# Optimization experiments

Measured on AMD Instinct MI355X. Metric: run time of the kernel, lower is better.

Reference implementation:

```python
import jax, jax.numpy as jnp
import numpy as np

SPC = 8                                   # samples_per_class
SIG_TEMP = 0.01                           # sigmoid_temperature
K_VALS = (1.0, 2.0, 4.0, 8.0, 16.0)       # all <= batch_size so min(batch,k)=k
K_TEMPS = (1.0, 2.0, 4.0, 8.0, 16.0)


def _sig(x, temp):
    # faithful to original: clamp exponent to [-50, 50]
    e = jnp.clip(-x / temp, -50.0, 50.0)
    return 1.0 / (1.0 + jnp.exp(e))


def setup_inputs() -> dict:
    key = jax.random.key(0)
    preds = jax.random.normal(key, (2048, 1024), dtype=jnp.float32)
    # embeddings are typically L2-normalized before this loss
    preds = preds / jnp.linalg.norm(preds, axis=1, keepdims=True)
    return {"preds": preds, "q_idx": 0}


def reference(preds, q_idx):
    B = preds.shape[0]
    spc = SPC
    kv = jnp.asarray(K_VALS, preds.dtype)          # [K]
    kt = jnp.asarray(K_TEMPS, preds.dtype)         # [K]
    norm_vals = jnp.minimum(kv, float(spc - 1))    # [K]

    idx = jnp.arange(B)
    g = idx // spc            # group id of each query
    r = idx % spc             # position of query within its group

    # all pairwise similarities: S[q, j] = <preds[q], preds[j]>
    S = preds @ preds.T                                        # [B, B]

    # G[q, i] = sim of query q with i-th member of q's own group
    cols = g[:, None] * spc + jnp.arange(spc)[None, :]         # [B, spc]
    G = jnp.take_along_axis(S, cols, axis=1)                   # [B, spc]

    # sim_diff_all[q, j, i] = S[q, j] - G[q, i]
    sg = _sig(S[:, :, None] - G[:, None, :], SIG_TEMP)         # [B, B, spc]

    # zero sim_sg[q, g(q)*spc + i, i]
    jr = jnp.arange(B)[None, :, None]
    ir = jnp.arange(spc)[None, None, :]
    diag_mask = jr == (g[:, None, None] * spc + ir)            # [B, B, spc]
    sg = jnp.where(diag_mask, 0.0, sg)

    # surrogate rank of each in-group sample w.r.t. query q
    rk = 1.0 + sg.sum(axis=1)                                  # [B, spc]
    self_mask = jnp.arange(spc)[None, :] == r[:, None]         # [B, spc]
    rk = jnp.where(self_mask, 0.0, rk)

    # per-k sigmoid indicator rank <= k
    v = _sig(kv[None, None, :] - rk[:, :, None], kt[None, None, :])  # [B, spc, K]
    v = jnp.where(self_mask[:, :, None], 0.0, v)

    recall = jnp.minimum(v.sum(axis=1), kv[None, :]) / norm_vals[None, :]  # [B, K]
    recall_q = recall.mean(axis=1)                                         # [B]
    return jnp.mean(1.0 - recall_q)
```

## Files before the change

### kernel.cpp

```cpp
#include <hip/hip_runtime.h>

#define BATCH 2048
#define DIM   1024
#define SPC   8
#define BM    128
#define BN    64
#define BK    32
#define NKT   (DIM / BK)
#define NJB   (BATCH / BN)

typedef _Float16 half8  __attribute__((ext_vector_type(8)));
typedef _Float16 half4v __attribute__((ext_vector_type(4)));
typedef float    f32x4  __attribute__((ext_vector_type(4)));

constexpr float INV_T    = 1.0f / 0.01f;
constexpr float LO_SCALE = 2048.0f;
constexpr float INV_LO   = 1.0f / 2048.0f;

__device__ __forceinline__ float sig_main(float x) {
  float e = -x * INV_T;
  e = fminf(fmaxf(e, -50.0f), 50.0f);
  return 1.0f / (1.0f + __expf(e));
}

__device__ __forceinline__ void gl_lds16(const _Float16* g, _Float16* l) {
  __builtin_amdgcn_global_load_lds((const __attribute__((address_space(1))) void*)g,
                                   (__attribute__((address_space(3))) void*)l, 16, 0, 0);
}

__device__ __forceinline__ int swz(int row, int c) { return row * 4 + (c ^ ((row >> 1) & 3)); }

__global__ __launch_bounds__(256) void k_prep(const float* __restrict__ preds,
                                              _Float16* __restrict__ Ph,
                                              _Float16* __restrict__ Pl,
                                              float* __restrict__ G) {
  __shared__ float rows[SPC][DIM + 4];
  __shared__ float part[64][4];
  if (blockIdx.x < BATCH) {
    const int i = blockIdx.x * 256 + threadIdx.x;
    const float4 x = ((const float4*)preds)[i];
    half4v h, l;
    h[0] = (_Float16)x.x; l[0] = (_Float16)((x.x - (float)h[0]) * LO_SCALE);
    h[1] = (_Float16)x.y; l[1] = (_Float16)((x.y - (float)h[1]) * LO_SCALE);
    h[2] = (_Float16)x.z; l[2] = (_Float16)((x.z - (float)h[2]) * LO_SCALE);
    h[3] = (_Float16)x.w; l[3] = (_Float16)((x.w - (float)h[3]) * LO_SCALE);
    ((half4v*)Ph)[i] = h;
    ((half4v*)Pl)[i] = l;
    return;
  }
  const int g = blockIdx.x - BATCH;
  const int tid = threadIdx.x;
  const float4* src = (const float4*)(preds + (size_t)g * SPC * DIM);
#pragma unroll
  for (int c = 0; c < 8; ++c) {
    int idx = c * 256 + tid;
    float4 v = src[idx];
    *(float4*)&rows[idx >> 8][(idx & 255) << 2] = v;
  }
  __syncthreads();
  const int p  = tid & 63;
  const int sl = tid >> 6;
  const float4* ra = (const float4*)&rows[p >> 3][sl * 256];
  const float4* rb = (const float4*)&rows[p & 7][sl * 256];
  float s = 0.0f;
#pragma unroll 8
  for (int e = 0; e < 64; ++e) {
    float4 a = ra[e], b = rb[e];
    s += a.x * b.x + a.y * b.y + a.z * b.z + a.w * b.w;
  }
  part[p][sl] = s;
  __syncthreads();
  if (tid < 64) {
    float v = part[tid][0] + part[tid][1] + part[tid][2] + part[tid][3];
    G[(size_t)(g * SPC + (tid >> 3)) * SPC + (tid & 7)] = v;
  }
}

__global__ __launch_bounds__(256, 2) void k_main(const _Float16* __restrict__ Ph,
                                                 const _Float16* __restrict__ Pl,
                                                 const float* __restrict__ G,
                                                 float* __restrict__ partial) {
  __shared__ __align__(16) _Float16 sAh0[BM * BK], sAl0[BM * BK], sBh0[BN * BK], sBl0[BN * BK];
  __shared__ __align__(16) _Float16 sAh1[BM * BK], sAl1[BM * BK], sBh1[BN * BK], sBl1[BN * BK];
  __shared__ float sRed[2][BM][SPC];
  const int t    = threadIdx.x;
  const int lane = t & 63;
  const int w    = t >> 6;
  const int wr   = w >> 1, wc = w & 1;

  int bid = blockIdx.y * gridDim.x + blockIdx.x;
  bid = (bid & 7) * (512 / 8) + (bid >> 3);
  const int qb    = (bid / NJB) * BM;
  const int jbIdx = bid % NJB;
  const int jb    = jbIdx * BN;

  f32x4 accH[4][2], accX[4][2];
#pragma unroll
  for (int m = 0; m < 4; ++m)
#pragma unroll
    for (int n = 0; n < 2; ++n) {
      accH[m][n] = (f32x4){0.f, 0.f, 0.f, 0.f};
      accX[m][n] = (f32x4){0.f, 0.f, 0.f, 0.f};
    }

  auto STAGE = [&](_Float16* dAh, _Float16* dAl, _Float16* dBh, _Float16* dBl, int kt) {
    const int kk = kt * BK;
#pragma unroll
    for (int e = 0; e < 2; ++e) {
      const int slot = e * 256 + t;
      const int row  = slot >> 2;
      const int c    = (slot & 3) ^ ((row >> 1) & 3);
      const size_t src = (size_t)(qb + row) * DIM + kk + c * 8;
      gl_lds16(Ph + src, dAh + (size_t)slot * 8);
      gl_lds16(Pl + src, dAl + (size_t)slot * 8);
    }
    {
      const int slot = t;
      const int row  = slot >> 2;
      const int c    = (slot & 3) ^ ((row >> 1) & 3);
      const size_t src = (size_t)(jb + row) * DIM + kk + c * 8;
      gl_lds16(Ph + src, dBh + (size_t)slot * 8);
      gl_lds16(Pl + src, dBl + (size_t)slot * 8);
    }
  };

  const int rl = lane & 15, ch = lane >> 4;
  auto COMPUTE = [&](const _Float16* bAh, const _Float16* bAl,
                     const _Float16* bBh, const _Float16* bBl) {
    half8 ah[4], al[4], bh[2], bl[2];
#pragma unroll
    for (int m = 0; m < 4; ++m) {
      const int r = wr * 64 + m * 16 + rl;
      const int s = swz(r, ch);
      ah[m] = *(const half8*)&bAh[(size_t)s * 8];
      al[m] = *(const half8*)&bAl[(size_t)s * 8];
    }
#pragma unroll
    for (int n = 0; n < 2; ++n) {
      const int r = wc * 32 + n * 16 + rl;
      const int s = swz(r, ch);
      bh[n] = *(const half8*)&bBh[(size_t)s * 8];
      bl[n] = *(const half8*)&bBl[(size_t)s * 8];
    }
#pragma unroll
    for (int m = 0; m < 4; ++m)
#pragma unroll
      for (int n = 0; n < 2; ++n) {
        accH[m][n] = __builtin_amdgcn_mfma_f32_16x16x32_f16(ah[m], bh[n], accH[m][n], 0, 0, 0);
        accX[m][n] = __builtin_amdgcn_mfma_f32_16x16x32_f16(ah[m], bl[n], accX[m][n], 0, 0, 0);
        accX[m][n] = __builtin_amdgcn_mfma_f32_16x16x32_f16(al[m], bh[n], accX[m][n], 0, 0, 0);
      }
  };

  STAGE(sAh0, sAl0, sBh0, sBl0, 0);
  __syncthreads();
#pragma unroll 1
  for (int kt = 0; kt < NKT; kt += 2) {
    if (kt + 1 < NKT) STAGE(sAh1, sAl1, sBh1, sBl1, kt + 1);
    COMPUTE(sAh0, sAl0, sBh0, sBl0);
    __syncthreads();
    if (kt + 2 < NKT) STAGE(sAh0, sAl0, sBh0, sBl0, kt + 2);
    COMPUTE(sAh1, sAl1, sBh1, sBl1);
    __syncthreads();
  }

  const int colLane = lane & 15;
  const int rowLane = lane >> 4;
#pragma unroll
  for (int m = 0; m < 4; ++m) {
#pragma unroll
    for (int v = 0; v < 4; ++v) {
      const int q = qb + wr * 64 + m * 16 + rowLane * 4 + v;
      const float4 g0 = *(const float4*)&G[(size_t)q * 8];
      const float4 g1 = *(const float4*)&G[(size_t)q * 8 + 4];
      const float gv[8] = {g0.x, g0.y, g0.z, g0.w, g1.x, g1.y, g1.z, g1.w};
      const int qg = q >> 3;
      float sv[2];
      int jg[2], jp[2];
#pragma unroll
      for (int n = 0; n < 2; ++n) {
        sv[n] = accH[m][n][v] + accX[m][n][v] * INV_LO;
        const int j = jb + wc * 32 + n * 16 + colLane;
        jg[n] = j >> 3;
        jp[n] = j & 7;
      }
#pragma unroll
      for (int i = 0; i < 8; ++i) {
        float pr = 0.0f;
#pragma unroll
        for (int n = 0; n < 2; ++n) {
          float s = sig_main(sv[n] - gv[i]);
          if (jg[n] == qg && jp[n] == i) s = 0.0f;
          pr += s;
        }
        pr += __shfl_xor(pr, 1);
        pr += __shfl_xor(pr, 2);
        pr += __shfl_xor(pr, 4);
        pr += __shfl_xor(pr, 8);
        if (colLane == 0)
          sRed[wc][wr * 64 + m * 16 + rowLane * 4 + v][i] = pr;
      }
    }
  }
  __syncthreads();
  {
    const float* r0 = &sRed[0][0][0];
    const float* r1 = &sRed[1][0][0];
    float4 a = *(const float4*)&r0[t * 4];
    float4 b = *(const float4*)&r1[t * 4];
    float4 s = {a.x + b.x, a.y + b.y, a.z + b.z, a.w + b.w};
    *(float4*)&partial[((size_t)jbIdx * BATCH + qb) * SPC + t * 4] = s;
  }
}

__global__ __launch_bounds__(256) void k_fin(const float* __restrict__ partial,
                                             float* __restrict__ out) {
  const int q = blockIdx.x * 256 + threadIdx.x;
  float rk8[8] = {0.f, 0.f, 0.f, 0.f, 0.f, 0.f, 0.f, 0.f};
#pragma unroll 4
  for (int p = 0; p < NJB; ++p) {
    const float* base = &partial[((size_t)p * BATCH + q) * SPC];
    float4 a = *(const float4*)&base[0];
    float4 b = *(const float4*)&base[4];
    rk8[0] += a.x; rk8[1] += a.y; rk8[2] += a.z; rk8[3] += a.w;
    rk8[4] += b.x; rk8[5] += b.y; rk8[6] += b.z; rk8[7] += b.w;
  }
  const float kv[5]  = {1.f, 2.f, 4.f, 8.f, 16.f};
  const float rkt[5] = {1.f, 0.5f, 0.25f, 0.125f, 0.0625f};
  const float nv[5]  = {1.f, 2.f, 4.f, 7.f, 7.f};
  const int r = q & 7;
  float vs[5] = {0.f, 0.f, 0.f, 0.f, 0.f};
#pragma unroll
  for (int i = 0; i < 8; ++i) {
    const float rk = 1.0f + rk8[i];
    const bool self = (i == r);
#pragma unroll
    for (int k = 0; k < 5; ++k) {
      float e = (rk - kv[k]) * rkt[k];
      e = fminf(fmaxf(e, -50.0f), 50.0f);
      float v = 1.0f / (1.0f + __expf(e));
      vs[k] += self ? 0.0f : v;
    }
  }
  float rq = 0.0f;
#pragma unroll
  for (int k = 0; k < 5; ++k) rq += fminf(vs[k], kv[k]) / nv[k];
  float tv = (1.0f - rq * 0.2f) * (1.0f / (float)BATCH);
#pragma unroll
  for (int o = 1; o < 64; o <<= 1) tv += __shfl_xor(tv, o);
  if ((threadIdx.x & 63) == 0) atomicAdd(out, tv);
}

extern "C" void kernel_launch(void* const* d_in, const int* in_sizes, int n_in,
                              void* d_out, int out_size, void* d_ws, size_t ws_size,
                              hipStream_t stream) {
  const float* preds = (const float*)d_in[0];
  float* G       = (float*)d_ws;
  float* partial = (float*)((char*)d_ws + (64 << 10));
  _Float16* Ph   = (_Float16*)((char*)d_ws + (64 << 10) + (2 << 20));
  _Float16* Pl   = Ph + (size_t)BATCH * DIM;
  hipMemsetAsync(d_out, 0, sizeof(float), stream);
  k_prep<<<BATCH + BATCH / SPC, 256, 0, stream>>>(preds, Ph, Pl, G);
  k_main<<<dim3(BATCH / BN, BATCH / BM), 256, 0, stream>>>(Ph, Pl, G, partial);
  k_fin<<<BATCH / 256, 256, 0, stream>>>(partial, (float*)d_out);
}
```

Before: 131.0 us.

## Shrink main tile to 64x64, remap blocks per XCD, parallelize final reduction

```diff
diff --git a/kernel.cpp b/kernel.cpp
--- a/kernel.cpp
+++ b/kernel.cpp
@@ -3,7 +3,7 @@
 #define BATCH 2048
 #define DIM   1024
 #define SPC   8
-#define BM    128
+#define BM    64
 #define BN    64
 #define BK    32
 #define NKT   (DIM / BK)
@@ -17,10 +17,9 @@
 constexpr float LO_SCALE = 2048.0f;
 constexpr float INV_LO   = 1.0f / 2048.0f;
 
-__device__ __forceinline__ float sig_main(float x) {
-  float e = -x * INV_T;
-  e = fminf(fmaxf(e, -50.0f), 50.0f);
-  return 1.0f / (1.0f + __expf(e));
+__device__ __forceinline__ float sig_fast(float x) {
+  float e = fminf(fmaxf(-x * INV_T, -50.0f), 50.0f);
+  return __builtin_amdgcn_rcpf(1.0f + __expf(e));
 }
 
 __device__ __forceinline__ void gl_lds16(const _Float16* g, _Float16* l) {
@@ -76,7 +75,7 @@
   }
 }
 
-__global__ __launch_bounds__(256, 2) void k_main(const _Float16* __restrict__ Ph,
+__global__ __launch_bounds__(256, 4) void k_main(const _Float16* __restrict__ Ph,
                                                  const _Float16* __restrict__ Pl,
                                                  const float* __restrict__ G,
                                                  float* __restrict__ partial) {
@@ -88,15 +87,15 @@
   const int w    = t >> 6;
   const int wr   = w >> 1, wc = w & 1;
 
-  int bid = blockIdx.y * gridDim.x + blockIdx.x;
-  bid = (bid & 7) * (512 / 8) + (bid >> 3);
-  const int qb    = (bid / NJB) * BM;
-  const int jbIdx = bid % NJB;
+  const int d    = blockIdx.y * 32 + blockIdx.x;
+  const int xcd  = d & 7, idx = d >> 3;
+  const int jbIdx = xcd * 4 + (idx & 3);
+  const int qb    = (idx >> 2) * BM;
   const int jb    = jbIdx * BN;
 
-  f32x4 accH[4][2], accX[4][2];
-#pragma unroll
-  for (int m = 0; m < 4; ++m)
+  f32x4 accH[2][2], accX[2][2];
+#pragma unroll
+  for (int m = 0; m < 2; ++m)
 #pragma unroll
     for (int n = 0; n < 2; ++n) {
       accH[m][n] = (f32x4){0.f, 0.f, 0.f, 0.f};
@@ -104,46 +103,35 @@
     }
 
   auto STAGE = [&](_Float16* dAh, _Float16* dAl, _Float16* dBh, _Float16* dBl, int kt) {
-    const int kk = kt * BK;
-#pragma unroll
-    for (int e = 0; e < 2; ++e) {
-      const int slot = e * 256 + t;
-      const int row  = slot >> 2;
-      const int c    = (slot & 3) ^ ((row >> 1) & 3);
-      const size_t src = (size_t)(qb + row) * DIM + kk + c * 8;
-      gl_lds16(Ph + src, dAh + (size_t)slot * 8);
-      gl_lds16(Pl + src, dAl + (size_t)slot * 8);
-    }
-    {
-      const int slot = t;
-      const int row  = slot >> 2;
-      const int c    = (slot & 3) ^ ((row >> 1) & 3);
-      const size_t src = (size_t)(jb + row) * DIM + kk + c * 8;
-      gl_lds16(Ph + src, dBh + (size_t)slot * 8);
-      gl_lds16(Pl + src, dBl + (size_t)slot * 8);
-    }
+    const int kk  = kt * BK;
+    const int row = t >> 2;
+    const int c   = (t & 3) ^ ((row >> 1) & 3);
+    const size_t sA = (size_t)(qb + row) * DIM + kk + c * 8;
+    const size_t sB = (size_t)(jb + row) * DIM + kk + c * 8;
+    gl_lds16(Ph + sA, dAh + (size_t)t * 8);
+    gl_lds16(Pl + sA, dAl + (size_t)t * 8);
+    gl_lds16(Ph + sB, dBh + (size_t)t * 8);
+    gl_lds16(Pl + sB, dBl + (size_t)t * 8);
   };
 
   const int rl = lane & 15, ch = lane >> 4;
   auto COMPUTE = [&](const _Float16* bAh, const _Float16* bAl,
                      const _Float16* bBh, const _Float16* bBl) {
-    half8 ah[4], al[4], bh[2], bl[2];
-#pragma unroll
-    for (int m = 0; m < 4; ++m) {
-      const int r = wr * 64 + m * 16 + rl;
-      const int s = swz(r, ch);
+    half8 ah[2], al[2], bh[2], bl[2];
+#pragma unroll
+    for (int m = 0; m < 2; ++m) {
+      const int s = swz(wr * 32 + m * 16 + rl, ch);
       ah[m] = *(const half8*)&bAh[(size_t)s * 8];
       al[m] = *(const half8*)&bAl[(size_t)s * 8];
     }
 #pragma unroll
     for (int n = 0; n < 2; ++n) {
-      const int r = wc * 32 + n * 16 + rl;
-      const int s = swz(r, ch);
+      const int s = swz(wc * 32 + n * 16 + rl, ch);
       bh[n] = *(const half8*)&bBh[(size_t)s * 8];
       bl[n] = *(const half8*)&bBl[(size_t)s * 8];
     }
 #pragma unroll
-    for (int m = 0; m < 4; ++m)
+    for (int m = 0; m < 2; ++m)
 #pragma unroll
       for (int n = 0; n < 2; ++n) {
         accH[m][n] = __builtin_amdgcn_mfma_f32_16x16x32_f16(ah[m], bh[n], accH[m][n], 0, 0, 0);
@@ -167,10 +155,11 @@
   const int colLane = lane & 15;
   const int rowLane = lane >> 4;
 #pragma unroll
-  for (int m = 0; m < 4; ++m) {
+  for (int m = 0; m < 2; ++m) {
 #pragma unroll
     for (int v = 0; v < 4; ++v) {
-      const int q = qb + wr * 64 + m * 16 + rowLane * 4 + v;
+      const int ql = wr * 32 + m * 16 + rowLane * 4 + v;
+      const int q  = qb + ql;
       const float4 g0 = *(const float4*)&G[(size_t)q * 8];
       const float4 g1 = *(const float4*)&G[(size_t)q * 8 + 4];
       const float gv[8] = {g0.x, g0.y, g0.z, g0.w, g1.x, g1.y, g1.z, g1.w};
@@ -189,7 +178,7 @@
         float pr = 0.0f;
 #pragma unroll
         for (int n = 0; n < 2; ++n) {
-          float s = sig_main(sv[n] - gv[i]);
+          float s = sig_fast(sv[n] - gv[i]);
           if (jg[n] == qg && jp[n] == i) s = 0.0f;
           pr += s;
         }
@@ -197,13 +186,12 @@
         pr += __shfl_xor(pr, 2);
         pr += __shfl_xor(pr, 4);
         pr += __shfl_xor(pr, 8);
-        if (colLane == 0)
-          sRed[wc][wr * 64 + m * 16 + rowLane * 4 + v][i] = pr;
+        if (colLane == 0) sRed[wc][ql][i] = pr;
       }
     }
   }
   __syncthreads();
-  {
+  if (t < 128) {
     const float* r0 = &sRed[0][0][0];
     const float* r1 = &sRed[1][0][0];
     float4 a = *(const float4*)&r0[t * 4];
@@ -215,40 +203,41 @@
 
 __global__ __launch_bounds__(256) void k_fin(const float* __restrict__ partial,
                                              float* __restrict__ out) {
-  const int q = blockIdx.x * 256 + threadIdx.x;
-  float rk8[8] = {0.f, 0.f, 0.f, 0.f, 0.f, 0.f, 0.f, 0.f};
-#pragma unroll 4
-  for (int p = 0; p < NJB; ++p) {
-    const float* base = &partial[((size_t)p * BATCH + q) * SPC];
-    float4 a = *(const float4*)&base[0];
-    float4 b = *(const float4*)&base[4];
-    rk8[0] += a.x; rk8[1] += a.y; rk8[2] += a.z; rk8[3] += a.w;
-    rk8[4] += b.x; rk8[5] += b.y; rk8[6] += b.z; rk8[7] += b.w;
-  }
+  const int tg = blockIdx.x * 256 + threadIdx.x;
+  const int q = tg >> 3, i = tg & 7;
+  float rk = 1.0f;
+#pragma unroll 8
+  for (int p = 0; p < NJB; ++p)
+    rk += partial[(size_t)p * BATCH * SPC + tg];
   const float kv[5]  = {1.f, 2.f, 4.f, 8.f, 16.f};
   const float rkt[5] = {1.f, 0.5f, 0.25f, 0.125f, 0.0625f};
   const float nv[5]  = {1.f, 2.f, 4.f, 7.f, 7.f};
-  const int r = q & 7;
-  float vs[5] = {0.f, 0.f, 0.f, 0.f, 0.f};
-#pragma unroll
-  for (int i = 0; i < 8; ++i) {
-    const float rk = 1.0f + rk8[i];
-    const bool self = (i == r);
-#pragma unroll
-    for (int k = 0; k < 5; ++k) {
-      float e = (rk - kv[k]) * rkt[k];
-      e = fminf(fmaxf(e, -50.0f), 50.0f);
-      float v = 1.0f / (1.0f + __expf(e));
-      vs[k] += self ? 0.0f : v;
-    }
-  }
-  float rq = 0.0f;
-#pragma unroll
-  for (int k = 0; k < 5; ++k) rq += fminf(vs[k], kv[k]) / nv[k];
-  float tv = (1.0f - rq * 0.2f) * (1.0f / (float)BATCH);
+  const bool self = (i == (q & 7));
+  float vs[5];
+#pragma unroll
+  for (int k = 0; k < 5; ++k) {
+    float e = (rk - kv[k]) * rkt[k];
+    e = fminf(fmaxf(e, -50.0f), 50.0f);
+    float v = 1.0f / (1.0f + __expf(e));
+    vs[k] = self ? 0.0f : v;
+  }
+#pragma unroll
+  for (int o = 1; o < 8; o <<= 1)
+#pragma unroll
+    for (int k = 0; k < 5; ++k) vs[k] += __shfl_xor(vs[k], o);
+  float tv = 0.0f;
+  if (i == 0) {
+    float rq = 0.0f;
+#pragma unroll
+    for (int k = 0; k < 5; ++k) rq += fminf(vs[k], kv[k]) / nv[k];
+    tv = (1.0f - rq * 0.2f) * (1.0f / (float)BATCH);
+  }
 #pragma unroll
   for (int o = 1; o < 64; o <<= 1) tv += __shfl_xor(tv, o);
-  if ((threadIdx.x & 63) == 0) atomicAdd(out, tv);
+  __shared__ float sw[4];
+  if ((threadIdx.x & 63) == 0) sw[threadIdx.x >> 6] = tv;
+  __syncthreads();
+  if (threadIdx.x == 0) atomicAdd(out, sw[0] + sw[1] + sw[2] + sw[3]);
 }
 
 extern "C" void kernel_launch(void* const* d_in, const int* in_sizes, int n_in,
@@ -261,6 +250,6 @@
   _Float16* Pl   = Ph + (size_t)BATCH * DIM;
   hipMemsetAsync(d_out, 0, sizeof(float), stream);
   k_prep<<<BATCH + BATCH / SPC, 256, 0, stream>>>(preds, Ph, Pl, G);
-  k_main<<<dim3(BATCH / BN, BATCH / BM), 256, 0, stream>>>(Ph, Pl, G, partial);
-  k_fin<<<BATCH / 256, 256, 0, stream>>>(partial, (float*)d_out);
-}
+  k_main<<<dim3(32, 32), 256, 0, stream>>>(Ph, Pl, G, partial);
+  k_fin<<<64, 256, 0, stream>>>(partial, (float*)d_out);
+}
```

After: 121.6 us. -7.1%, faster.
